# Kernel tuning notes

Hardware: AMD Instinct MI355X
Metric: run time of the kernel (lower is better)

The kernel has to match this reference:

```python
import jax, jax.numpy as jnp
import numpy as np

TOP_K = 12
OBS_RADIUS = 1.0
DIST_MIN_THRES = 0.8
EPS = 1e-4


def setup_inputs() -> dict:
    key = jax.random.key(0)
    ks = jax.random.split(key, 9)
    N, in_dim = 4096, 4
    c = in_dim + 2  # pairwise diff + eye flag + (dist - thres)
    states = jax.random.normal(ks[0], (N, in_dim), dtype=jnp.float32) * 2.0
    def w(k, o, i):
        return jax.random.normal(k, (o, i), dtype=jnp.float32) * (1.0 / np.sqrt(i))
    return {
        "states": states,
        "W1": w(ks[1], 64, c),  "b1": jnp.zeros((64,), jnp.float32),
        "W2": w(ks[2], 128, 64), "b2": jnp.zeros((128,), jnp.float32),
        "W3": w(ks[3], 64, 128), "b3": jnp.zeros((64,), jnp.float32),
        "W4": w(ks[4], 1, 64),   "b4": jnp.zeros((1,), jnp.float32),
    }


def _conv1x1(h, W, b):
    # h: [N, C_in, L]; 1x1 Conv1d == channel matmul
    return jnp.einsum('oi,nil->nol', W, h) + b[None, :, None]


def reference(states, W1, b1, W2, b2, W3, b3, W4, b4):
    N = states.shape[0]
    # pairwise differences: [N, N, in_dim]
    x = states[:, None, :] - states[None, :, :]
    d_norm = jnp.sqrt(jnp.sum(jnp.square(x[:, :, :2]) + EPS, axis=2))  # [N, N]
    eye = jnp.eye(N, dtype=x.dtype)
    x = jnp.concatenate(
        [x, eye[:, :, None], (d_norm - DIST_MIN_THRES)[:, :, None]], axis=2
    )  # [N, N, c]
    # remove_distant_agents: keep TOP_K nearest neighbors per agent
    dn = jnp.sqrt(jnp.sum(jnp.square(x[:, :, :2]) + EPS, axis=2))  # [N, N]
    _, idx = jax.lax.top_k(-dn, TOP_K)                              # [N, k]
    x = jnp.take_along_axis(x, idx[:, :, None], axis=1)            # [N, k, c]
    dist = jnp.sqrt(jnp.sum(jnp.square(x[:, :, :2]) + EPS, axis=2, keepdims=True))  # [N,k,1]
    k, c = x.shape[1], x.shape[2]
    mask = (dist <= OBS_RADIUS).astype(x.dtype).reshape(-1, 1, k)  # [N,1,k] (reshape, as in source)
    h = x.reshape(-1, c, k)  # faithful: source uses reshape, NOT transpose
    h = jax.nn.relu(_conv1x1(h, W1, b1))
    h = jax.nn.relu(_conv1x1(h, W2, b2))
    h = jax.nn.relu(_conv1x1(h, W3, b3))
    h = _conv1x1(h, W4, b4)  # [N, 1, k]
    h = h * mask
    return h, mask
```

## Files before the change

### kernel.cpp

```cpp
#include <hip/hip_runtime.h>
#include <stdint.h>

#define NAG 4096
#define TOPK 12
#define EPSF 1e-4f
#define NT 256
#define PT (NAG / NT)
#define MTOT (NAG * TOPK)

typedef unsigned long long u64;
typedef short short8v __attribute__((ext_vector_type(8)));
typedef float f32x4 __attribute__((ext_vector_type(4)));

__device__ __forceinline__ u64 umin64(u64 a, u64 b) { return a < b ? a : b; }

__device__ __forceinline__ unsigned short f2bf(float f) {
    union { float f; unsigned u; } v; v.f = f;
    unsigned r = v.u + 0x7FFFu + ((v.u >> 16) & 1u);
    return (unsigned short)(r >> 16);
}

__global__ __launch_bounds__(NT, 8)
void cbf_select(const float* __restrict__ states,
                float* __restrict__ xbuf,
                float* __restrict__ out)
{
    const int i = blockIdx.x;
    const int t = threadIdx.x;
    const int lane = t & 63;
    const int wv = t >> 6;

    __shared__ float s_dn[NT * 17];
    __shared__ u64 s_min[NT];
    __shared__ int s_sel[TOPK];
    __shared__ float s_x[72];

    const float2* st2 = reinterpret_cast<const float2*>(states);
    const float si0 = states[i * 4 + 0];
    const float si1 = states[i * 4 + 1];

    float mind = 1e30f;
    int minu = 0;
#pragma unroll
    for (int u = 0; u < PT; ++u) {
        int j = u * NT + t;
        float2 sj = st2[j * 2];
        float dx0 = __fsub_rn(si0, sj.x);
        float dx1 = __fsub_rn(si1, sj.y);
        float d2 = __fadd_rn(__fadd_rn(__fmul_rn(dx0, dx0), EPSF),
                             __fadd_rn(__fmul_rn(dx1, dx1), EPSF));
        float dn = __fsqrt_rn(d2);
        s_dn[t * 17 + u] = dn;
        if (dn < mind) { mind = dn; minu = u; }
    }
    s_min[t] = ((u64)__float_as_uint(mind) << 32) | (unsigned)(minu * NT + t);
    __syncthreads();

    if (wv == 0) {
        volatile u64* vmin = s_min;
        volatile float* vdn = s_dn;
        for (int r = 0; r < TOPK; ++r) {
            u64 m = umin64(umin64(vmin[lane], vmin[lane + 64]),
                           umin64(vmin[lane + 128], vmin[lane + 192]));
#pragma unroll
            for (int off = 32; off > 0; off >>= 1)
                m = umin64(m, (u64)__shfl_xor((unsigned long long)m, off, 64));
            int j = (int)(unsigned)(m & 0xffffffffull);
            int tp = j & (NT - 1);
            if (lane == 0) {
                s_sel[r] = j;
                vdn[tp * 17 + (j >> 8)] = 1e30f;
            }
            __builtin_amdgcn_wave_barrier();
            int u2 = lane & 15;
            float d = vdn[tp * 17 + u2];
            u64 km = ((u64)__float_as_uint(d) << 32) | (unsigned)(u2 * NT + tp);
#pragma unroll
            for (int off = 8; off > 0; off >>= 1)
                km = umin64(km, (u64)__shfl_xor((unsigned long long)km, off, 64));
            if (lane == 0) vmin[tp] = km;
            __builtin_amdgcn_wave_barrier();
        }
    }
    __syncthreads();

    if (t < TOPK) {
        int j = s_sel[t];
        const float4 sj = reinterpret_cast<const float4*>(states)[j];
        const float4 si = reinterpret_cast<const float4*>(states)[i];
        float dx0 = __fsub_rn(si.x, sj.x);
        float dx1 = __fsub_rn(si.y, sj.y);
        float dx2 = __fsub_rn(si.z, sj.z);
        float dx3 = __fsub_rn(si.w, sj.w);
        float d2 = __fadd_rn(__fadd_rn(__fmul_rn(dx0, dx0), EPSF),
                             __fadd_rn(__fmul_rn(dx1, dx1), EPSF));
        float dn = __fsqrt_rn(d2);
        s_x[t * 6 + 0] = dx0;
        s_x[t * 6 + 1] = dx1;
        s_x[t * 6 + 2] = dx2;
        s_x[t * 6 + 3] = dx3;
        s_x[t * 6 + 4] = (j == i) ? 1.0f : 0.0f;
        s_x[t * 6 + 5] = __fsub_rn(dn, 0.8f);
        out[MTOT + i * TOPK + t] = (dn <= 1.0f) ? 1.0f : 0.0f;
    }
    __syncthreads();

    if (t < TOPK) {
        int m = i * TOPK + t;
        float4 v0 = {s_x[0 * 12 + t], s_x[1 * 12 + t], s_x[2 * 12 + t], s_x[3 * 12 + t]};
        float4 v1 = {s_x[4 * 12 + t], s_x[5 * 12 + t], 0.0f, 0.0f};
        reinterpret_cast<float4*>(xbuf + m * 8)[0] = v0;
        reinterpret_cast<float4*>(xbuf + m * 8)[1] = v1;
    }
}

__global__ __launch_bounds__(256)
void cbf_mlp(const float* __restrict__ xbuf,
             const float* __restrict__ W1, const float* __restrict__ b1,
             const float* __restrict__ W2, const float* __restrict__ b2,
             const float* __restrict__ W3, const float* __restrict__ b3,
             const float* __restrict__ W4, const float* __restrict__ b4,
             float* __restrict__ out)
{
    const int t = threadIdx.x;
    const int lane = t & 63;
    const int wv = t >> 6;
    const int r16 = lane & 15;
    const int hi = lane >> 4;
    const int m0 = blockIdx.x * 64 + wv * 16;

    __shared__ __align__(16) unsigned char s_h1[4 * 2048];
    __shared__ __align__(16) unsigned char s_h2[4 * 4096];
    unsigned char* lp1 = s_h1 + wv * 2048;
    unsigned char* lp2 = s_h2 + wv * 4096;

    const int mrow = m0 + r16;
    const float4 xa = reinterpret_cast<const float4*>(xbuf + mrow * 8)[0];
    const float4 xb = reinterpret_cast<const float4*>(xbuf + mrow * 8)[1];
    const float xc[6] = {xa.x, xa.y, xa.z, xa.w, xb.x, xb.y};

    unsigned short h1b[16];
#pragma unroll
    for (int ol = 0; ol < 16; ++ol) {
        int o = hi * 16 + ol;
        const float2* wr = reinterpret_cast<const float2*>(W1 + o * 6);
        float2 w0 = wr[0], w1 = wr[1], w2 = wr[2];
        float acc = b1[o];
        acc = fmaf(w0.x, xc[0], acc);
        acc = fmaf(w0.y, xc[1], acc);
        acc = fmaf(w1.x, xc[2], acc);
        acc = fmaf(w1.y, xc[3], acc);
        acc = fmaf(w2.x, xc[4], acc);
        acc = fmaf(w2.y, xc[5], acc);
        h1b[ol] = f2bf(fmaxf(acc, 0.0f));
    }
    {
        short8v p0, p1;
#pragma unroll
        for (int e = 0; e < 8; ++e) { p0[e] = (short)h1b[e]; p1[e] = (short)h1b[8 + e]; }
        int rowb = r16 * 128;
        *(short8v*)(lp1 + rowb + (((2 * hi + 0) ^ (r16 & 7)) * 16)) = p0;
        *(short8v*)(lp1 + rowb + (((2 * hi + 1) ^ (r16 & 7)) * 16)) = p1;
    }
    __syncthreads();

    short8v a0 = *(short8v*)(lp1 + r16 * 128 + (((0 + hi) ^ (r16 & 7)) * 16));
    short8v a1 = *(short8v*)(lp1 + r16 * 128 + (((4 + hi) ^ (r16 & 7)) * 16));
    const int c = r16;
#pragma unroll
    for (int nt = 0; nt < 8; ++nt) {
        const float* wrow = W2 + (nt * 16 + c) * 64;
        float4 g0 = *(const float4*)(wrow + 8 * hi);
        float4 g1 = *(const float4*)(wrow + 8 * hi + 4);
        float4 g2 = *(const float4*)(wrow + 32 + 8 * hi);
        float4 g3 = *(const float4*)(wrow + 36 + 8 * hi);
        short8v bf0, bf1;
        bf0[0] = (short)f2bf(g0.x); bf0[1] = (short)f2bf(g0.y);
        bf0[2] = (short)f2bf(g0.z); bf0[3] = (short)f2bf(g0.w);
        bf0[4] = (short)f2bf(g1.x); bf0[5] = (short)f2bf(g1.y);
        bf0[6] = (short)f2bf(g1.z); bf0[7] = (short)f2bf(g1.w);
        bf1[0] = (short)f2bf(g2.x); bf1[1] = (short)f2bf(g2.y);
        bf1[2] = (short)f2bf(g2.z); bf1[3] = (short)f2bf(g2.w);
        bf1[4] = (short)f2bf(g3.x); bf1[5] = (short)f2bf(g3.y);
        bf1[6] = (short)f2bf(g3.z); bf1[7] = (short)f2bf(g3.w);
        float bb = b2[nt * 16 + c];
        f32x4 acc = {bb, bb, bb, bb};
        acc = __builtin_amdgcn_mfma_f32_16x16x32_bf16(a0, bf0, acc, 0, 0, 0);
        acc = __builtin_amdgcn_mfma_f32_16x16x32_bf16(a1, bf1, acc, 0, 0, 0);
#pragma unroll
        for (int e = 0; e < 4; ++e) {
            unsigned short hv = f2bf(fmaxf(acc[e], 0.0f));
            int mr = 4 * hi + e;
            int slot = (2 * nt + (c >> 3)) ^ (mr & 15);
            *(unsigned short*)(lp2 + mr * 256 + slot * 16 + ((2 * c) & 15)) = hv;
        }
    }
    __syncthreads();

    short8v a3[4];
#pragma unroll
    for (int ks = 0; ks < 4; ++ks)
        a3[ks] = *(short8v*)(lp2 + r16 * 256 + (((4 * ks + hi) ^ r16) * 16));
    float h3r[4][4];
#pragma unroll
    for (int nt = 0; nt < 4; ++nt) {
        const float* wrow = W3 + (nt * 16 + c) * 128;
        float bb = b3[nt * 16 + c];
        f32x4 ac = {bb, bb, bb, bb};
#pragma unroll
        for (int ks = 0; ks < 4; ++ks) {
            float4 q0 = *(const float4*)(wrow + ks * 32 + 8 * hi);
            float4 q1 = *(const float4*)(wrow + ks * 32 + 8 * hi + 4);
            short8v bf;
            bf[0] = (short)f2bf(q0.x); bf[1] = (short)f2bf(q0.y);
            bf[2] = (short)f2bf(q0.z); bf[3] = (short)f2bf(q0.w);
            bf[4] = (short)f2bf(q1.x); bf[5] = (short)f2bf(q1.y);
            bf[6] = (short)f2bf(q1.z); bf[7] = (short)f2bf(q1.w);
            ac = __builtin_amdgcn_mfma_f32_16x16x32_bf16(a3[ks], bf, ac, 0, 0, 0);
        }
#pragma unroll
        for (int e = 0; e < 4; ++e) h3r[nt][e] = fmaxf(ac[e], 0.0f);
    }

    float w4c[4];
#pragma unroll
    for (int nt = 0; nt < 4; ++nt) w4c[nt] = W4[nt * 16 + c];
    float part[4];
#pragma unroll
    for (int e = 0; e < 4; ++e) {
        float p = h3r[0][e] * w4c[0];
        p = fmaf(h3r[1][e], w4c[1], p);
        p = fmaf(h3r[2][e], w4c[2], p);
        p = fmaf(h3r[3][e], w4c[3], p);
        part[e] = p;
    }
#pragma unroll
    for (int off = 1; off <= 8; off <<= 1) {
#pragma unroll
        for (int e = 0; e < 4; ++e)
            part[e] += __shfl_xor(part[e], off, 64);
    }
    if (c == 0) {
        float bb4 = b4[0];
#pragma unroll
        for (int e = 0; e < 4; ++e) {
            int m = m0 + 4 * hi + e;
            float mk = out[MTOT + m];
            out[m] = (part[e] + bb4) * mk;
        }
    }
}

extern "C" void kernel_launch(void* const* d_in, const int* in_sizes, int n_in,
                              void* d_out, int out_size, void* d_ws, size_t ws_size,
                              hipStream_t stream) {
    const float* states = (const float*)d_in[0];
    const float* W1 = (const float*)d_in[1];
    const float* b1 = (const float*)d_in[2];
    const float* W2 = (const float*)d_in[3];
    const float* b2 = (const float*)d_in[4];
    const float* W3 = (const float*)d_in[5];
    const float* b3 = (const float*)d_in[6];
    const float* W4 = (const float*)d_in[7];
    const float* b4 = (const float*)d_in[8];
    float* out = (float*)d_out;
    float* xbuf = (float*)d_ws;

    cbf_select<<<dim3(NAG), dim3(NT), 0, stream>>>(states, xbuf, out);
    cbf_mlp<<<dim3(MTOT / 64), dim3(256), 0, stream>>>(xbuf, W1, b1, W2, b2,
                                                       W3, b3, W4, b4, out);
}
```

Baseline: 122.4 us.

## Keep top-k candidate minima in registers and reduce with DPP instead of shuffles

The top-k selection loop in wave 0 now holds the 256 per-thread minimum keys in registers (4 per lane) instead of re-reading shared memory each round. The cross-lane argmin uses DPP row operations plus a readlane in place of __shfl_xor butterflies. The refresh of the chosen thread's column minimum is done by every lane with a 16-entry register reduction, replacing the shuffle-based one and its wave barriers. This aims to cut LDS traffic and shuffle latency on the serial 12-round critical path, at the cost of more registers and redundant per-lane work.

```diff
diff --git a/kernel.cpp b/kernel.cpp
--- a/kernel.cpp
+++ b/kernel.cpp
@@ -18,6 +18,15 @@
     union { float f; unsigned u; } v; v.f = f;
     unsigned r = v.u + 0x7FFFu + ((v.u >> 16) & 1u);
     return (unsigned short)(r >> 16);
+}
+
+template <int CTRL>
+__device__ __forceinline__ void dpp_min_step(unsigned &hi, unsigned &lo) {
+    unsigned ohi = (unsigned)__builtin_amdgcn_update_dpp((int)hi, (int)hi, CTRL, 0xf, 0xf, false);
+    unsigned olo = (unsigned)__builtin_amdgcn_update_dpp((int)lo, (int)lo, CTRL, 0xf, 0xf, false);
+    bool t = (ohi < hi) || (ohi == hi && olo < lo);
+    hi = t ? ohi : hi;
+    lo = t ? olo : lo;
 }
 
 __global__ __launch_bounds__(NT, 8)
@@ -57,29 +66,57 @@
     __syncthreads();
 
     if (wv == 0) {
-        volatile u64* vmin = s_min;
-        volatile float* vdn = s_dn;
+        unsigned khi[4], klo[4];
+#pragma unroll
+        for (int q = 0; q < 4; ++q) {
+            u64 kk = s_min[lane + q * 64];
+            klo[q] = (unsigned)(kk & 0xffffffffull);
+            khi[q] = (unsigned)(kk >> 32);
+        }
         for (int r = 0; r < TOPK; ++r) {
-            u64 m = umin64(umin64(vmin[lane], vmin[lane + 64]),
-                           umin64(vmin[lane + 128], vmin[lane + 192]));
-#pragma unroll
-            for (int off = 32; off > 0; off >>= 1)
-                m = umin64(m, (u64)__shfl_xor((unsigned long long)m, off, 64));
-            int j = (int)(unsigned)(m & 0xffffffffull);
-            int tp = j & (NT - 1);
+            unsigned hi = khi[0], lo = klo[0];
+#pragma unroll
+            for (int q = 1; q < 4; ++q) {
+                bool tk = (khi[q] < hi) || (khi[q] == hi && klo[q] < lo);
+                hi = tk ? khi[q] : hi;
+                lo = tk ? klo[q] : lo;
+            }
+            dpp_min_step<0xB1>(hi, lo);
+            dpp_min_step<0x4E>(hi, lo);
+            dpp_min_step<0x124>(hi, lo);
+            dpp_min_step<0x128>(hi, lo);
+            dpp_min_step<0x142>(hi, lo);
+            dpp_min_step<0x143>(hi, lo);
+            int j = __builtin_amdgcn_readlane((int)lo, 63);
+            int gp = j & (NT - 1);
+            int uw = j >> 8;
             if (lane == 0) {
                 s_sel[r] = j;
-                vdn[tp * 17 + (j >> 8)] = 1e30f;
+                s_dn[gp * 17 + uw] = 1e30f;
             }
-            __builtin_amdgcn_wave_barrier();
-            int u2 = lane & 15;
-            float d = vdn[tp * 17 + u2];
-            u64 km = ((u64)__float_as_uint(d) << 32) | (unsigned)(u2 * NT + tp);
-#pragma unroll
-            for (int off = 8; off > 0; off >>= 1)
-                km = umin64(km, (u64)__shfl_xor((unsigned long long)km, off, 64));
-            if (lane == 0) vmin[tp] = km;
-            __builtin_amdgcn_wave_barrier();
+            u64 kv[16];
+#pragma unroll
+            for (int u = 0; u < 16; ++u) {
+                float d = s_dn[gp * 17 + u];
+                d = (u == uw) ? 1e30f : d;
+                kv[u] = ((u64)__float_as_uint(d) << 4) | (unsigned)u;
+            }
+#pragma unroll
+            for (int st = 8; st > 0; st >>= 1)
+#pragma unroll
+                for (int q = 0; q < 8; ++q)
+                    if (q < st) kv[q] = umin64(kv[q], kv[q + st]);
+            unsigned numin = (unsigned)(kv[0] & 15ull);
+            unsigned nhi = (unsigned)(kv[0] >> 4);
+            unsigned nlo = numin * NT + (unsigned)gp;
+            bool own = (gp & 63) == lane;
+            int idx = gp >> 6;
+#pragma unroll
+            for (int q = 0; q < 4; ++q) {
+                bool w = own && (idx == q);
+                khi[q] = w ? nhi : khi[q];
+                klo[q] = w ? nlo : klo[q];
+            }
         }
     }
     __syncthreads();
```

Measured after the change: 124.1 us. No clear change (+1.3%).

## Use one wavefront per agent with register-resident distances and threshold-based top-k

Applied to the files above, without the earlier changes.

Each wavefront now handles one agent, so a block covers four agents. Each lane keeps its 64 distances in registers instead of shared memory. A 12-round DPP min reduction finds the 12th-smallest distance as a threshold. Ballot compaction then gathers the survivors into shared memory, and a rank-by-count pass orders them. This drops block-wide syncs and most shared-memory traffic, but uses many more registers (launch bounds lowered to 4) and caps survivors at 64, which is only safe if ties stay few.

```diff
diff --git a/kernel.cpp b/kernel.cpp
--- a/kernel.cpp
+++ b/kernel.cpp
@@ -5,7 +5,7 @@
 #define TOPK 12
 #define EPSF 1e-4f
 #define NT 256
-#define PT (NAG / NT)
+#define WPB 4
 #define MTOT (NAG * TOPK)
 
 typedef unsigned long long u64;
@@ -20,72 +20,97 @@
     return (unsigned short)(r >> 16);
 }
 
-__global__ __launch_bounds__(NT, 8)
+template <int CTRL>
+__device__ __forceinline__ void dpp_min_step(unsigned &hi, unsigned &lo) {
+    unsigned ohi = (unsigned)__builtin_amdgcn_update_dpp((int)hi, (int)hi, CTRL, 0xf, 0xf, false);
+    unsigned olo = (unsigned)__builtin_amdgcn_update_dpp((int)lo, (int)lo, CTRL, 0xf, 0xf, false);
+    bool t = (ohi < hi) || (ohi == hi && olo < lo);
+    hi = t ? ohi : hi;
+    lo = t ? olo : lo;
+}
+
+__global__ __launch_bounds__(NT, 4)
 void cbf_select(const float* __restrict__ states,
                 float* __restrict__ xbuf,
                 float* __restrict__ out)
 {
-    const int i = blockIdx.x;
     const int t = threadIdx.x;
     const int lane = t & 63;
     const int wv = t >> 6;
-
-    __shared__ float s_dn[NT * 17];
-    __shared__ u64 s_min[NT];
-    __shared__ int s_sel[TOPK];
-    __shared__ float s_x[72];
+    const int i = blockIdx.x * WPB + wv;
+
+    __shared__ u64 s_surv[WPB][64];
+    __shared__ int s_sel[WPB][TOPK];
+    __shared__ float s_x[WPB][72];
 
     const float2* st2 = reinterpret_cast<const float2*>(states);
     const float si0 = states[i * 4 + 0];
     const float si1 = states[i * 4 + 1];
 
-    float mind = 1e30f;
-    int minu = 0;
-#pragma unroll
-    for (int u = 0; u < PT; ++u) {
-        int j = u * NT + t;
+    unsigned dnb[64];
+    unsigned minb = 0xFFFFFFFFu;
+    int minj = 0;
+#pragma unroll
+    for (int u = 0; u < 64; ++u) {
+        int j = u * 64 + lane;
         float2 sj = st2[j * 2];
         float dx0 = __fsub_rn(si0, sj.x);
         float dx1 = __fsub_rn(si1, sj.y);
         float d2 = __fadd_rn(__fadd_rn(__fmul_rn(dx0, dx0), EPSF),
                              __fadd_rn(__fmul_rn(dx1, dx1), EPSF));
-        float dn = __fsqrt_rn(d2);
-        s_dn[t * 17 + u] = dn;
-        if (dn < mind) { mind = dn; minu = u; }
-    }
-    s_min[t] = ((u64)__float_as_uint(mind) << 32) | (unsigned)(minu * NT + t);
-    __syncthreads();
-
-    if (wv == 0) {
-        volatile u64* vmin = s_min;
-        volatile float* vdn = s_dn;
+        unsigned b = __float_as_uint(__fsqrt_rn(d2));
+        dnb[u] = b;
+        if (b < minb) { minb = b; minj = j; }
+    }
+
+    unsigned Tb;
+    {
+        unsigned khi = minb, klo = (unsigned)minj;
+        unsigned Tcur = 0;
         for (int r = 0; r < TOPK; ++r) {
-            u64 m = umin64(umin64(vmin[lane], vmin[lane + 64]),
-                           umin64(vmin[lane + 128], vmin[lane + 192]));
-#pragma unroll
-            for (int off = 32; off > 0; off >>= 1)
-                m = umin64(m, (u64)__shfl_xor((unsigned long long)m, off, 64));
-            int j = (int)(unsigned)(m & 0xffffffffull);
-            int tp = j & (NT - 1);
-            if (lane == 0) {
-                s_sel[r] = j;
-                vdn[tp * 17 + (j >> 8)] = 1e30f;
-            }
-            __builtin_amdgcn_wave_barrier();
-            int u2 = lane & 15;
-            float d = vdn[tp * 17 + u2];
-            u64 km = ((u64)__float_as_uint(d) << 32) | (unsigned)(u2 * NT + tp);
-#pragma unroll
-            for (int off = 8; off > 0; off >>= 1)
-                km = umin64(km, (u64)__shfl_xor((unsigned long long)km, off, 64));
-            if (lane == 0) vmin[tp] = km;
-            __builtin_amdgcn_wave_barrier();
-        }
-    }
-    __syncthreads();
-
-    if (t < TOPK) {
-        int j = s_sel[t];
+            unsigned hi = khi, lo = klo;
+            dpp_min_step<0xB1>(hi, lo);
+            dpp_min_step<0x4E>(hi, lo);
+            dpp_min_step<0x124>(hi, lo);
+            dpp_min_step<0x128>(hi, lo);
+            dpp_min_step<0x142>(hi, lo);
+            dpp_min_step<0x143>(hi, lo);
+            unsigned hw = (unsigned)__builtin_amdgcn_readlane((int)hi, 63);
+            unsigned lw = (unsigned)__builtin_amdgcn_readlane((int)lo, 63);
+            Tcur = hw;
+            if (khi == hw && klo == lw) khi = 0xFFFFFFFFu;
+        }
+        Tb = Tcur;
+    }
+
+    int cnt = 0;
+#pragma unroll
+    for (int u = 0; u < 64; ++u) {
+        bool p = (dnb[u] <= Tb);
+        u64 mk = __ballot(p);
+        if (p) {
+            int pos = cnt + __popcll(mk & ((1ull << lane) - 1ull));
+            if (pos < 64)
+                s_surv[wv][pos] = ((u64)dnb[u] << 32) | (unsigned)(u * 64 + lane);
+        }
+        cnt += __popcll(mk);
+    }
+    if (cnt > 64) cnt = 64;
+    __asm volatile("s_waitcnt lgkmcnt(0)" ::: "memory");
+    __builtin_amdgcn_wave_barrier();
+
+    if (lane < cnt) {
+        u64 kA = s_surv[wv][lane];
+        int rA = 0;
+        for (int q = 0; q < cnt; ++q)
+            rA += (s_surv[wv][q] < kA) ? 1 : 0;
+        if (rA < TOPK) s_sel[wv][rA] = (int)(unsigned)(kA & 0xffffffffull);
+    }
+    __asm volatile("s_waitcnt lgkmcnt(0)" ::: "memory");
+    __builtin_amdgcn_wave_barrier();
+
+    if (lane < TOPK) {
+        int j = s_sel[wv][lane];
         const float4 sj = reinterpret_cast<const float4*>(states)[j];
         const float4 si = reinterpret_cast<const float4*>(states)[i];
         float dx0 = __fsub_rn(si.x, sj.x);
@@ -95,20 +120,22 @@
         float d2 = __fadd_rn(__fadd_rn(__fmul_rn(dx0, dx0), EPSF),
                              __fadd_rn(__fmul_rn(dx1, dx1), EPSF));
         float dn = __fsqrt_rn(d2);
-        s_x[t * 6 + 0] = dx0;
-        s_x[t * 6 + 1] = dx1;
-        s_x[t * 6 + 2] = dx2;
-        s_x[t * 6 + 3] = dx3;
-        s_x[t * 6 + 4] = (j == i) ? 1.0f : 0.0f;
-        s_x[t * 6 + 5] = __fsub_rn(dn, 0.8f);
-        out[MTOT + i * TOPK + t] = (dn <= 1.0f) ? 1.0f : 0.0f;
-    }
-    __syncthreads();
-
-    if (t < TOPK) {
-        int m = i * TOPK + t;
-        float4 v0 = {s_x[0 * 12 + t], s_x[1 * 12 + t], s_x[2 * 12 + t], s_x[3 * 12 + t]};
-        float4 v1 = {s_x[4 * 12 + t], s_x[5 * 12 + t], 0.0f, 0.0f};
+        s_x[wv][lane * 6 + 0] = dx0;
+        s_x[wv][lane * 6 + 1] = dx1;
+        s_x[wv][lane * 6 + 2] = dx2;
+        s_x[wv][lane * 6 + 3] = dx3;
+        s_x[wv][lane * 6 + 4] = (j == i) ? 1.0f : 0.0f;
+        s_x[wv][lane * 6 + 5] = __fsub_rn(dn, 0.8f);
+        out[MTOT + i * TOPK + lane] = (dn <= 1.0f) ? 1.0f : 0.0f;
+    }
+    __asm volatile("s_waitcnt lgkmcnt(0)" ::: "memory");
+    __builtin_amdgcn_wave_barrier();
+
+    if (lane < TOPK) {
+        int m = i * TOPK + lane;
+        float4 v0 = {s_x[wv][0 * 12 + lane], s_x[wv][1 * 12 + lane],
+                     s_x[wv][2 * 12 + lane], s_x[wv][3 * 12 + lane]};
+        float4 v1 = {s_x[wv][4 * 12 + lane], s_x[wv][5 * 12 + lane], 0.0f, 0.0f};
         reinterpret_cast<float4*>(xbuf + m * 8)[0] = v0;
         reinterpret_cast<float4*>(xbuf + m * 8)[1] = v1;
     }
@@ -266,7 +293,7 @@
     float* out = (float*)d_out;
     float* xbuf = (float*)d_ws;
 
-    cbf_select<<<dim3(NAG), dim3(NT), 0, stream>>>(states, xbuf, out);
+    cbf_select<<<dim3(NAG / WPB), dim3(NT), 0, stream>>>(states, xbuf, out);
     cbf_mlp<<<dim3(MTOT / 64), dim3(256), 0, stream>>>(xbuf, W1, b1, W2, b2,
                                                        W3, b3, W4, b4, out);
 }
```

Measured after the change: 122.7 us. About the same (+0.2%).
